# Performance work log

Measured on AMD Instinct MI355X. Metric: run time of the kernel, lower is better.

## Reference

```python
import jax, jax.numpy as jnp
from jax import lax
import numpy as np

B = 32768
H = 7
W = 7
EMB = 64
NUM_ACTIONS = 7
HIDDEN = 128
CNN_OUT = 64 * 3 * 3  # 576, from 7x7 input through the conv/pool stack


def setup_inputs() -> dict:
    key = jax.random.key(0)
    ks = jax.random.split(key, 20)
    frame = jax.random.randint(ks[0], (2, B, H, W, 3), 0, 11, dtype=jnp.int32)
    carried_col = jax.random.randint(ks[1], (2, B, 1), 0, 6, dtype=jnp.int32)
    carried_obj = jax.random.randint(ks[2], (2, B, 1), 0, 11, dtype=jnp.int32)

    def w(k, shape):
        return (jax.random.normal(k, shape, jnp.float32) * 0.05)

    return {
        "frame": frame,
        "carried_col": carried_col,
        "carried_obj": carried_obj,
        "conv1_w": w(ks[3], (16, 3, 2, 2)),  "conv1_b": jnp.zeros((16,), jnp.float32),
        "conv2_w": w(ks[4], (32, 16, 2, 2)), "conv2_b": jnp.zeros((32,), jnp.float32),
        "conv3_w": w(ks[5], (64, 32, 2, 2)), "conv3_b": jnp.zeros((64,), jnp.float32),
        "proj_w": w(ks[6], (EMB, CNN_OUT + 2)), "proj_b": jnp.zeros((EMB,), jnp.float32),
        "h1_w": w(ks[7], (HIDDEN, EMB * 2 + 4)), "h1_b": jnp.zeros((HIDDEN,), jnp.float32),
        "ln_g": jnp.ones((HIDDEN,), jnp.float32), "ln_b": jnp.zeros((HIDDEN,), jnp.float32),
        "h2_w": w(ks[8], (HIDDEN, HIDDEN)), "h2_b": jnp.zeros((HIDDEN,), jnp.float32),
        "h3_w": w(ks[9], (NUM_ACTIONS, HIDDEN)), "h3_b": jnp.zeros((NUM_ACTIONS,), jnp.float32),
    }


def _conv(x, wgt, b):
    # Conv2d(kernel=2, padding=1), NCHW
    y = lax.conv_general_dilated(x, wgt, (1, 1), [(1, 1), (1, 1)],
                                 dimension_numbers=("NCHW", "OIHW", "NCHW"))
    return y + b[None, :, None, None]


def _maxpool2(x):
    # MaxPool2d(2): window 2, stride 2, floor (VALID)
    return lax.reduce_window(x, -jnp.inf, lax.max, (1, 1, 2, 2), (1, 1, 2, 2), "VALID")


def _encode(fr, cc, co, p):
    x = fr.transpose(0, 3, 1, 2).astype(jnp.float32)  # [B,3,H,W]
    x = _maxpool2(jax.nn.relu(_conv(x, p["conv1_w"], p["conv1_b"])))  # [B,16,4,4]
    x = _maxpool2(jax.nn.relu(_conv(x, p["conv2_w"], p["conv2_b"])))  # [B,32,2,2]
    x = jax.nn.relu(_conv(x, p["conv3_w"], p["conv3_b"]))             # [B,64,3,3]
    feats = x.reshape(x.shape[0], -1)                                  # [B,576]
    carried = jnp.concatenate([cc, co], axis=-1).astype(jnp.float32)   # [B,2]
    comb = jnp.concatenate([feats, carried], axis=1)                   # [B,578]
    return jax.nn.relu(comb @ p["proj_w"].T + p["proj_b"])            # [B,64]


def _dir_pos(fr):
    # vectorized first-match of frame[...,0]==10 in row-major order
    b = fr.shape[0]
    mask = (fr[..., 0] == 10).reshape(b, -1)             # [B, H*W]
    has = jnp.any(mask, axis=-1)                         # [B]
    idx = jnp.argmax(mask, axis=-1)                      # first True (row-major)
    y = idx // W
    x = idx % W
    ch2 = fr[..., 2].reshape(b, -1)
    d_raw = jnp.take_along_axis(ch2, idx[:, None], axis=1)[:, 0] % 4
    d = jnp.where(has, d_raw, 0)                         # [B] int
    pos = jnp.stack([y.astype(jnp.float32) / (H - 1),
                     x.astype(jnp.float32) / (W - 1)], axis=-1)
    pos = jnp.where(has[:, None], pos, jnp.float32(0.5))  # [B,2]
    return d, pos


def _forward(frame, carried_col, carried_obj, p):
    curr_f, next_f = frame[0], frame[1]
    curr_emb = _encode(curr_f, carried_col[0], carried_obj[0], p)
    next_emb = _encode(next_f, carried_col[1], carried_obj[1], p)
    cd, cpos = _dir_pos(curr_f)
    nd, npos = _dir_pos(next_f)
    delta = ((nd - cd + 4) % 4).astype(jnp.float32)
    angle = delta * (2.0 * 3.14159 / 4.0)  # matches source constant
    dir_delta = jnp.stack([jnp.sin(angle), jnp.cos(angle)], axis=-1)  # [B,2]
    pos_delta = npos - cpos                                           # [B,2]
    comb = jnp.concatenate([curr_emb, next_emb, dir_delta, pos_delta], axis=-1)  # [B,132]
    h = comb @ p["h1_w"].T + p["h1_b"]
    mu = h.mean(-1, keepdims=True)
    var = ((h - mu) ** 2).mean(-1, keepdims=True)
    h = (h - mu) * lax.rsqrt(var + 1e-5) * p["ln_g"] + p["ln_b"]
    h = jax.nn.relu(h)  # dropout = identity in eval
    h = jax.nn.relu(h @ p["h2_w"].T + p["h2_b"])
    return h @ p["h3_w"].T + p["h3_b"]  # [B, num_actions]


def reference(frame, carried_col, carried_obj,
              conv1_w, conv1_b, conv2_w, conv2_b, conv3_w, conv3_b,
              proj_w, proj_b, h1_w, h1_b, ln_g, ln_b,
              h2_w, h2_b, h3_w, h3_b):
    p = dict(conv1_w=conv1_w, conv1_b=conv1_b, conv2_w=conv2_w, conv2_b=conv2_b,
             conv3_w=conv3_w, conv3_b=conv3_b, proj_w=proj_w, proj_b=proj_b,
             h1_w=h1_w, h1_b=h1_b, ln_g=ln_g, ln_b=ln_b,
             h2_w=h2_w, h2_b=h2_b, h3_w=h3_w, h3_b=h3_b)
    return _forward(frame, carried_col, carried_obj, p)
```

## Files before the change

kernel.cpp:

```cpp
#include <hip/hip_runtime.h>
#include <hip/hip_bf16.h>

#define BATCH 32768
#define NELEM 65536

typedef unsigned short u16;
typedef unsigned int u32;
typedef __attribute__((ext_vector_type(8))) short bf16x8;
typedef __attribute__((ext_vector_type(4))) float f32x4;

__device__ __forceinline__ float bf2f(u16 u) {
    union { u32 u; float f; } c; c.u = ((u32)u) << 16; return c.f;
}
__device__ __forceinline__ u16 f2bf(float f) {
    union { float f; u32 u; } c; c.f = f;
    u32 x = c.u;
    u32 r = (x + 0x7fffu + ((x >> 16) & 1u)) >> 16;
    return (u16)r;
}

__global__ __launch_bounds__(256) void k0_prep(const float* __restrict__ pw,
        const float* __restrict__ w2, const float* __restrict__ w3,
        const float* __restrict__ h2w, const float* __restrict__ h1w,
        const float* __restrict__ w1,
        u16* __restrict__ pwT, u16* __restrict__ w2r, u16* __restrict__ w3r,
        u16* __restrict__ h2hi, u16* __restrict__ h2lo,
        u16* __restrict__ h1hi, u16* __restrict__ h1lo,
        u16* __restrict__ w1hi, u16* __restrict__ w1lo) {
    int idx = blockIdx.x * 256 + threadIdx.x;
    if (idx < 38912) {
        int j = idx / 608, kk = idx - j * 608;
        float v = 0.f;
        if (kk < 576) {
            int p = kk >> 6, oc = kk & 63;
            v = pw[j * 578 + oc * 9 + p];
        } else if (kk < 578) {
            v = pw[j * 578 + kk];
        }
        pwT[idx] = f2bf(v);
    } else if (idx < 40960) {
        int i = idx - 38912;
        int oc = i >> 6, rem = i & 63, tap = rem >> 4, ic = rem & 15;
        w2r[i] = f2bf(w2[oc * 64 + ic * 4 + tap]);
    } else if (idx < 49152) {
        int i = idx - 40960;
        int oc = i >> 7, rem = i & 127, tap = rem >> 5, ic = rem & 31;
        w3r[i] = f2bf(w3[oc * 128 + ic * 4 + tap]);
    } else if (idx < 65536) {
        int i = idx - 49152;
        float v = h2w[i];
        u16 hi = f2bf(v);
        h2hi[i] = hi;
        h2lo[i] = f2bf(v - bf2f(hi));
    } else if (idx < 86016) {
        int i = idx - 65536;
        int j = i / 160, k = i - j * 160;
        float v = (k < 132) ? h1w[j * 132 + k] : 0.f;
        u16 hi = f2bf(v);
        h1hi[i] = hi;
        h1lo[i] = f2bf(v - bf2f(hi));
    } else if (idx < 86528) {
        int i = idx - 86016;
        int oc = i >> 5, k = i & 31;
        int ky = k >> 4, kx = (k >> 3) & 1, c = k & 7;
        float v = (c < 3) ? w1[oc * 12 + c * 4 + ky * 2 + kx] : 0.f;
        u16 hi = f2bf(v);
        w1hi[i] = hi;
        w1lo[i] = f2bf(v - bf2f(hi));
    }
}

__global__ __launch_bounds__(256) void k1_conv1_mfma(const int* __restrict__ frame,
        const u16* __restrict__ w1hi, const u16* __restrict__ w1lo,
        const float* __restrict__ b1, u16* __restrict__ pooled1b) {
    __shared__ u16 fr[16 * 656];
    int t = threadIdx.x;
    int e0 = blockIdx.x * 16;
    #pragma unroll
    for (int i = 0; i < 6; ++i) {
        int o = i * 256 + t;
        if (o < 1312) *(uint4*)(fr + o * 8) = make_uint4(0u, 0u, 0u, 0u);
    }
    __syncthreads();
    #pragma unroll
    for (int i = 0; i < 10; ++i) {
        int idx = i * 256 + t;
        if (idx < 2352) {
            int le = idx / 147, r = idx - le * 147;
            int cell = r / 3, c = r - cell * 3;
            int y = cell / 7, x = cell - y * 7;
            fr[le * 656 + (y + 1) * 72 + (x + 1) * 8 + c] = f2bf((float)frame[e0 * 147 + idx]);
        }
    }
    __syncthreads();
    int l = t & 63;
    int wv = t >> 6;
    int col = l & 15;
    int kg = l >> 4;
    bf16x8 bhi = *(const bf16x8*)(w1hi + col * 32 + kg * 8);
    bf16x8 blo = *(const bf16x8*)(w1lo + col * 32 + kg * 8);
    float bias = b1[col];
    int ky = kg >> 1, kx = kg & 1;
    bool writer = (kg < 2);
    #pragma unroll
    for (int q = 0; q < 4; ++q) {
        int le = wv * 4 + q;
        const u16* eb = fr + le * 656;
        u16* op = pooled1b + (size_t)(e0 + le) * 256;
        #pragma unroll
        for (int mt = 0; mt < 4; ++mt) {
            int posA = mt * 16 + col;
            int oy = posA >> 3, ox = posA & 7;
            bf16x8 a = *(const bf16x8*)(eb + (oy + ky) * 72 + (ox + kx) * 8);
            f32x4 acc = {0.f, 0.f, 0.f, 0.f};
            acc = __builtin_amdgcn_mfma_f32_16x16x32_bf16(a, bhi, acc, 0, 0, 0);
            acc = __builtin_amdgcn_mfma_f32_16x16x32_bf16(a, blo, acc, 0, 0, 0);
            float x0 = fmaxf(acc[0] + bias, 0.f);
            float x1 = fmaxf(acc[1] + bias, 0.f);
            float x2 = fmaxf(acc[2] + bias, 0.f);
            float x3 = fmaxf(acc[3] + bias, 0.f);
            float y0 = fmaxf(x0, x1);
            float y1 = fmaxf(x2, x3);
            float m0 = fmaxf(y0, __shfl_xor(y0, 32, 64));
            float m1 = fmaxf(y1, __shfl_xor(y1, 32, 64));
            if (writer) {
                op[(mt * 4 + kg * 2 + 0) * 16 + col] = f2bf(m0);
                op[(mt * 4 + kg * 2 + 1) * 16 + col] = f2bf(m1);
            }
        }
    }
}

#define K2_WAVES 4096
__global__ __launch_bounds__(256) void k2_conv2_mfma(const u16* __restrict__ pooled1b,
        const u16* __restrict__ w2r, const float* __restrict__ b2,
        u16* __restrict__ pooled2) {
    int t = threadIdx.x;
    int l = t & 63;
    int col = l & 15;
    int kg = l >> 4;
    int wv = (blockIdx.x * 256 + t) >> 6;

    bf16x8 bfrag[2][2];
    #pragma unroll
    for (int s = 0; s < 2; ++s)
        #pragma unroll
        for (int nt = 0; nt < 2; ++nt)
            bfrag[s][nt] = *(const bf16x8*)(w2r + (nt * 16 + col) * 64 + s * 32 + kg * 8);
    float bias[2] = { b2[col], b2[16 + col] };

    int oy = col >> 2, ox = col & 3;
    int aoff[2]; bool aok[2];
    #pragma unroll
    for (int s = 0; s < 2; ++s) {
        int tap = 2 * s + (kg >> 1);
        int ky = tap >> 1, kx = tap & 1;
        int iy = oy - 1 + ky, ix = ox - 1 + kx;
        aok[s] = (iy >= 0 && ix >= 0);
        aoff[s] = (iy * 4 + ix) * 16 + (kg & 1) * 8;
    }

    for (int e = wv; e < NELEM; e += K2_WAVES) {
        const u16* pbase = pooled1b + e * 256;
        bf16x8 a0 = {0,0,0,0,0,0,0,0}, a1 = {0,0,0,0,0,0,0,0};
        if (aok[0]) a0 = *(const bf16x8*)(pbase + aoff[0]);
        if (aok[1]) a1 = *(const bf16x8*)(pbase + aoff[1]);
        f32x4 acc0 = {0.f,0.f,0.f,0.f}, acc1 = {0.f,0.f,0.f,0.f};
        acc0 = __builtin_amdgcn_mfma_f32_16x16x32_bf16(a0, bfrag[0][0], acc0, 0, 0, 0);
        acc1 = __builtin_amdgcn_mfma_f32_16x16x32_bf16(a0, bfrag[0][1], acc1, 0, 0, 0);
        acc0 = __builtin_amdgcn_mfma_f32_16x16x32_bf16(a1, bfrag[1][0], acc0, 0, 0, 0);
        acc1 = __builtin_amdgcn_mfma_f32_16x16x32_bf16(a1, bfrag[1][1], acc1, 0, 0, 0);
        #pragma unroll
        for (int nt = 0; nt < 2; ++nt) {
            f32x4 acc = nt ? acc1 : acc0;
            float b = bias[nt];
            float m0 = fmaxf(fmaxf(acc[0] + b, 0.f), fmaxf(acc[1] + b, 0.f));
            float m1 = fmaxf(fmaxf(acc[2] + b, 0.f), fmaxf(acc[3] + b, 0.f));
            float p0 = fmaxf(m0, __shfl_xor(m0, 16, 64));
            float p1 = fmaxf(m1, __shfl_xor(m1, 16, 64));
            if ((kg & 1) == 0) {
                int q = (kg >> 1) * 2;
                u16* op = pooled2 + e * 128 + nt * 16 + col;
                op[q * 32]       = f2bf(p0);
                op[(q + 1) * 32] = f2bf(p1);
            }
        }
    }
}

__global__ __launch_bounds__(256) void k34_conv3_proj(const u16* __restrict__ pooled2,
        const u16* __restrict__ w3r, const float* __restrict__ b3,
        const int* __restrict__ ccol, const int* __restrict__ cobj,
        const u16* __restrict__ pwT, const float* __restrict__ pb,
        float* __restrict__ comb) {
    __shared__ u16 featL[32 * 640];
    __shared__ u16 p2L[32 * 128];
    int t = threadIdx.x;
    int l = t & 63;
    int col = l & 15;
    int kg = l >> 4;
    int wv = t >> 6;
    int e0 = blockIdx.x * 32;
    int colhi = col >> 3, collo = col & 7;

    {
        const uint4* src = (const uint4*)(pooled2 + (size_t)e0 * 128);
        uint4* dst = (uint4*)p2L;
        #pragma unroll
        for (int i = 0; i < 2; ++i) dst[i * 256 + t] = src[i * 256 + t];
    }
    __syncthreads();

    {
        bf16x8 bfrag[4][4];
        #pragma unroll
        for (int s = 0; s < 4; ++s)
            #pragma unroll
            for (int nt = 0; nt < 4; ++nt)
                bfrag[s][nt] = *(const bf16x8*)(w3r + (nt * 16 + col) * 128 + s * 32 + kg * 8);
        float bias[4];
        #pragma unroll
        for (int nt = 0; nt < 4; ++nt) bias[nt] = b3[nt * 16 + col];

        auto do_tile = [&](int i) {
            int m0 = i * 16;
            int m = m0 + col;
            u32 elem = (u32)(((unsigned long long)(u32)m * 954437177ull) >> 33);
            int p = m - (int)elem * 9;
            int oy = (p * 86) >> 8;
            int ox = p - 3 * oy;
            const u16* pbase = p2L + elem * 128 + kg * 8;
            f32x4 acc[4];
            #pragma unroll
            for (int nt = 0; nt < 4; ++nt) {
                acc[nt][0] = 0.f; acc[nt][1] = 0.f; acc[nt][2] = 0.f; acc[nt][3] = 0.f;
            }
            #pragma unroll
            for (int s = 0; s < 4; ++s) {
                int ky = s >> 1, kx = s & 1;
                int iy = oy - 1 + ky, ix = ox - 1 + kx;
                bf16x8 a = {0,0,0,0,0,0,0,0};
                if (iy >= 0 && iy <= 1 && ix >= 0 && ix <= 1)
                    a = *(const bf16x8*)(pbase + (iy * 2 + ix) * 32);
                #pragma unroll
                for (int nt = 0; nt < 4; ++nt)
                    acc[nt] = __builtin_amdgcn_mfma_f32_16x16x32_bf16(a, bfrag[s][nt], acc[nt], 0, 0, 0);
            }
            #pragma unroll
            for (int r = 0; r < 4; ++r) {
                int mr = m0 + kg * 4 + r;
                u32 er = (u32)(((unsigned long long)(u32)mr * 954437177ull) >> 33);
                int pr = mr - (int)er * 9;
                int e7 = (int)(er & 7u);
                u16* fb = featL + er * 640 + collo;
                #pragma unroll
                for (int nt = 0; nt < 4; ++nt) {
                    int blk = (pr * 8 + nt * 2 + colhi) ^ e7;
                    fb[blk * 8] = f2bf(fmaxf(acc[nt][r] + bias[nt], 0.f));
                }
            }
        };
        #pragma unroll
        for (int u = 0; u < 4; ++u) do_tile(wv + u * 4);
        if (wv < 2) do_tile(16 + wv);
    }
    if (t < 32) {
        union { u16 s[8]; uint4 q; } b;
        b.s[0] = f2bf((float)ccol[e0 + t]);
        b.s[1] = f2bf((float)cobj[e0 + t]);
        #pragma unroll
        for (int i = 2; i < 8; ++i) b.s[i] = 0;
        *(uint4*)(featL + t * 640 + (72 ^ (t & 7)) * 8) = b.q;
    }
    __syncthreads();

    int rh = wv & 1, nh = wv >> 1;
    int m0g = e0 + rh * 16;
    const u16* arowb = featL + (rh * 16 + col) * 640;
    int rx = col & 7;
    const u16* brow = pwT + (nh * 32 + col) * 608 + kg * 8;
    f32x4 acc0 = {0.f,0.f,0.f,0.f}, acc1 = {0.f,0.f,0.f,0.f};
    #pragma unroll
    for (int k0 = 0; k0 < 608; k0 += 32) {
        bf16x8 a;
        if (k0 + kg * 8 < 584) {
            int L = (k0 >> 3) + kg;
            a = *(const bf16x8*)(arowb + (L ^ rx) * 8);
        } else {
            #pragma unroll
            for (int j = 0; j < 8; ++j) a[j] = 0;
        }
        bf16x8 b0 = *(const bf16x8*)(brow + k0);
        bf16x8 b1 = *(const bf16x8*)(brow + 16 * 608 + k0);
        acc0 = __builtin_amdgcn_mfma_f32_16x16x32_bf16(a, b0, acc0, 0, 0, 0);
        acc1 = __builtin_amdgcn_mfma_f32_16x16x32_bf16(a, b1, acc1, 0, 0, 0);
    }
    float* outbase = (m0g < BATCH) ? (comb + (size_t)m0g * 160)
                                   : (comb + (size_t)(m0g - BATCH) * 160 + 64);
    #pragma unroll
    for (int nt = 0; nt < 2; ++nt) {
        int n = nh * 32 + nt * 16 + col;
        float pbv = pb[n];
        f32x4 acc = nt ? acc1 : acc0;
        #pragma unroll
        for (int r = 0; r < 4; ++r) {
            outbase[(kg * 4 + r) * 160 + n] = fmaxf(acc[r] + pbv, 0.f);
        }
    }
}

__global__ __launch_bounds__(256) void k5_extras(const int* __restrict__ frame,
        float* __restrict__ comb) {
    int b = blockIdx.x * 256 + threadIdx.x;
    int d[2]; float posy[2], posx[2];
    for (int f = 0; f < 2; ++f) {
        const int* fb = frame + (size_t)(f * BATCH + b) * 147;
        int idx = 49;
        for (int cell = 0; cell < 49; ++cell) {
            int v = fb[cell * 3];
            if (idx == 49 && v == 10) idx = cell;
        }
        if (idx < 49) {
            d[f] = fb[idx * 3 + 2] & 3;
            posy[f] = (float)(idx / 7) / 6.0f;
            posx[f] = (float)(idx % 7) / 6.0f;
        } else {
            d[f] = 0; posy[f] = 0.5f; posx[f] = 0.5f;
        }
    }
    int delta = (d[1] - d[0] + 4) & 3;
    const float ANG = (float)(2.0 * 3.14159 / 4.0);
    float angle = (float)delta * ANG;
    float4 o;
    o.x = sinf(angle);
    o.y = cosf(angle);
    o.z = posy[1] - posy[0];
    o.w = posx[1] - posx[0];
    float* cb = comb + (size_t)b * 160 + 128;
    *(float4*)cb = o;
    float4 z = make_float4(0.f, 0.f, 0.f, 0.f);
    #pragma unroll
    for (int i = 1; i < 8; ++i) *(float4*)(cb + i * 4) = z;
}

__device__ __forceinline__ void split8(const float* __restrict__ x,
                                       bf16x8& hi, bf16x8& lo) {
    #pragma unroll
    for (int j = 0; j < 8; ++j) {
        u16 h = f2bf(x[j]);
        hi[j] = (short)h;
        lo[j] = (short)f2bf(x[j] - bf2f(h));
    }
}

__global__ __launch_bounds__(256) void k6_h1_gemm(const float* __restrict__ in,
        const u16* __restrict__ whi, const u16* __restrict__ wlo,
        const float* __restrict__ bias, float* __restrict__ out) {
    int t = threadIdx.x;
    int l = t & 63;
    int col = l & 15;
    int kg = l >> 4;
    int m0 = blockIdx.x * 64 + (t >> 6) * 16;
    const float* arow = in + (size_t)(m0 + col) * 160 + kg * 8;
    const u16* bh = whi + col * 160 + kg * 8;
    const u16* bl = wlo + col * 160 + kg * 8;

    f32x4 acc[8];
    #pragma unroll
    for (int nt = 0; nt < 8; ++nt) {
        acc[nt][0] = 0.f; acc[nt][1] = 0.f; acc[nt][2] = 0.f; acc[nt][3] = 0.f;
    }
    #pragma unroll
    for (int s = 0; s < 5; ++s) {
        float x[8];
        #pragma unroll
        for (int j = 0; j < 8; ++j) x[j] = arow[s * 32 + j];
        bf16x8 ahi, alo;
        split8(x, ahi, alo);
        #pragma unroll
        for (int nt = 0; nt < 8; ++nt) {
            bf16x8 bhiF = *(const bf16x8*)(bh + nt * 2560 + s * 32);
            bf16x8 bloF = *(const bf16x8*)(bl + nt * 2560 + s * 32);
            acc[nt] = __builtin_amdgcn_mfma_f32_16x16x32_bf16(ahi, bhiF, acc[nt], 0, 0, 0);
            acc[nt] = __builtin_amdgcn_mfma_f32_16x16x32_bf16(alo, bhiF, acc[nt], 0, 0, 0);
            acc[nt] = __builtin_amdgcn_mfma_f32_16x16x32_bf16(ahi, bloF, acc[nt], 0, 0, 0);
        }
    }
    #pragma unroll
    for (int nt = 0; nt < 8; ++nt) {
        float bv = bias[nt * 16 + col];
        #pragma unroll
        for (int r = 0; r < 4; ++r) {
            int m = m0 + kg * 4 + r;
            out[m * 128 + nt * 16 + col] = acc[nt][r] + bv;
        }
    }
}

__global__ __launch_bounds__(256) void k6_ln(const float* __restrict__ h,
        const float* __restrict__ lng, const float* __restrict__ lnb,
        float* __restrict__ out) {
    int w = (blockIdx.x * 256 + threadIdx.x) >> 6;
    int l = threadIdx.x & 63;
    const float* row = h + (size_t)w * 128 + l * 2;
    float2 v = *(const float2*)row;
    float s = v.x + v.y;
    s += __shfl_xor(s, 1, 64);
    s += __shfl_xor(s, 2, 64);
    s += __shfl_xor(s, 4, 64);
    s += __shfl_xor(s, 8, 64);
    s += __shfl_xor(s, 16, 64);
    s += __shfl_xor(s, 32, 64);
    float mu = s * (1.0f / 128.0f);
    float d0 = v.x - mu, d1 = v.y - mu;
    float vs = d0 * d0 + d1 * d1;
    vs += __shfl_xor(vs, 1, 64);
    vs += __shfl_xor(vs, 2, 64);
    vs += __shfl_xor(vs, 4, 64);
    vs += __shfl_xor(vs, 8, 64);
    vs += __shfl_xor(vs, 16, 64);
    vs += __shfl_xor(vs, 32, 64);
    float rs = rsqrtf(vs * (1.0f / 128.0f) + 1e-5f);
    float2 o;
    o.x = fmaxf(d0 * rs * lng[l * 2]     + lnb[l * 2],     0.f);
    o.y = fmaxf(d1 * rs * lng[l * 2 + 1] + lnb[l * 2 + 1], 0.f);
    *(float2*)(out + (size_t)w * 128 + l * 2) = o;
}

__global__ __launch_bounds__(256) void k7_h2_mfma(const float* __restrict__ in,
        const u16* __restrict__ whi, const u16* __restrict__ wlo,
        const float* __restrict__ bias, float* __restrict__ out) {
    int t = threadIdx.x;
    int l = t & 63;
    int col = l & 15;
    int kg = l >> 4;
    int m0 = blockIdx.x * 64 + (t >> 6) * 16;
    const float* arow = in + (size_t)(m0 + col) * 128 + kg * 8;
    const u16* bh = whi + col * 128 + kg * 8;
    const u16* bl = wlo + col * 128 + kg * 8;

    f32x4 acc[8];
    #pragma unroll
    for (int nt = 0; nt < 8; ++nt) {
        acc[nt][0] = 0.f; acc[nt][1] = 0.f; acc[nt][2] = 0.f; acc[nt][3] = 0.f;
    }
    #pragma unroll
    for (int s = 0; s < 4; ++s) {
        float x[8];
        #pragma unroll
        for (int j = 0; j < 8; ++j) x[j] = arow[s * 32 + j];
        bf16x8 ahi, alo;
        split8(x, ahi, alo);
        #pragma unroll
        for (int nt = 0; nt < 8; ++nt) {
            bf16x8 bhiF = *(const bf16x8*)(bh + nt * 2048 + s * 32);
            bf16x8 bloF = *(const bf16x8*)(bl + nt * 2048 + s * 32);
            acc[nt] = __builtin_amdgcn_mfma_f32_16x16x32_bf16(ahi, bhiF, acc[nt], 0, 0, 0);
            acc[nt] = __builtin_amdgcn_mfma_f32_16x16x32_bf16(alo, bhiF, acc[nt], 0, 0, 0);
            acc[nt] = __builtin_amdgcn_mfma_f32_16x16x32_bf16(ahi, bloF, acc[nt], 0, 0, 0);
        }
    }
    #pragma unroll
    for (int nt = 0; nt < 8; ++nt) {
        float bv = bias[nt * 16 + col];
        #pragma unroll
        for (int r = 0; r < 4; ++r) {
            int m = m0 + kg * 4 + r;
            out[m * 128 + nt * 16 + col] = fmaxf(acc[nt][r] + bv, 0.f);
        }
    }
}

__global__ __launch_bounds__(256) void k8_h3(const float* __restrict__ in,
        const float* __restrict__ w, const float* __restrict__ bias,
        float* __restrict__ out) {
    int r = blockIdx.x * 256 + threadIdx.x;
    float acc[7];
    #pragma unroll
    for (int j = 0; j < 7; ++j) acc[j] = bias[j];
    const float* row = in + (size_t)r * 128;
    #pragma unroll 4
    for (int c = 0; c < 32; ++c) {
        float4 v = *(const float4*)(row + c * 4);
        #pragma unroll
        for (int j = 0; j < 7; ++j) {
            acc[j] += v.x * w[j * 128 + c * 4 + 0];
            acc[j] += v.y * w[j * 128 + c * 4 + 1];
            acc[j] += v.z * w[j * 128 + c * 4 + 2];
            acc[j] += v.w * w[j * 128 + c * 4 + 3];
        }
    }
    #pragma unroll
    for (int j = 0; j < 7; ++j) out[r * 7 + j] = acc[j];
}

extern "C" void kernel_launch(void* const* d_in, const int* in_sizes, int n_in,
                              void* d_out, int out_size, void* d_ws, size_t ws_size,
                              hipStream_t stream) {
    const int*   frame = (const int*)d_in[0];
    const int*   ccol  = (const int*)d_in[1];
    const int*   cobj  = (const int*)d_in[2];
    const float* w1    = (const float*)d_in[3];
    const float* b1    = (const float*)d_in[4];
    const float* w2    = (const float*)d_in[5];
    const float* b2    = (const float*)d_in[6];
    const float* w3    = (const float*)d_in[7];
    const float* b3    = (const float*)d_in[8];
    const float* pw    = (const float*)d_in[9];
    const float* pb    = (const float*)d_in[10];
    const float* h1w   = (const float*)d_in[11];
    const float* h1b   = (const float*)d_in[12];
    const float* lng   = (const float*)d_in[13];
    const float* lnb   = (const float*)d_in[14];
    const float* h2w   = (const float*)d_in[15];
    const float* h2b   = (const float*)d_in[16];
    const float* h3w   = (const float*)d_in[17];
    const float* h3b   = (const float*)d_in[18];
    float* out = (float*)d_out;

    char* ws = (char*)d_ws;
    u16*   pooled1b = (u16*)(ws + 0);
    float* comb     = (float*)(ws + 0);
    u16*   pooled2  = (u16*)(ws + 33554432);
    float* h1out    = (float*)(ws + 33554432);
    float* h2out    = (float*)(ws + 50331648);
    float* h1pre    = (float*)(ws + 95420416);
    u16*   pwT      = (u16*)(ws + 132120576);
    u16*   w2r      = (u16*)(ws + 132120576 + 131072);
    u16*   w3r      = (u16*)(ws + 132120576 + 139264);
    u16*   h2hi     = (u16*)(ws + 132120576 + 163840);
    u16*   h2lo     = (u16*)(ws + 132120576 + 196608);
    u16*   h1hi     = (u16*)(ws + 132120576 + 229376);
    u16*   h1lo     = (u16*)(ws + 132120576 + 270336);
    u16*   w1hi     = (u16*)(ws + 132120576 + 311296);
    u16*   w1lo     = (u16*)(ws + 132120576 + 312320);

    k0_prep<<<340, 256, 0, stream>>>(pw, w2, w3, h2w, h1w, w1,
                                     pwT, w2r, w3r, h2hi, h2lo, h1hi, h1lo,
                                     w1hi, w1lo);
    k1_conv1_mfma<<<4096, 256, 0, stream>>>(frame, w1hi, w1lo, b1, pooled1b);
    k2_conv2_mfma<<<1024, 256, 0, stream>>>(pooled1b, w2r, b2, pooled2);
    k34_conv3_proj<<<2048, 256, 0, stream>>>(pooled2, w3r, b3, ccol, cobj,
                                             pwT, pb, comb);
    k5_extras<<<128, 256, 0, stream>>>(frame, comb);
    k6_h1_gemm<<<512, 256, 0, stream>>>(comb, h1hi, h1lo, h1b, h1pre);
    k6_ln<<<8192, 256, 0, stream>>>(h1pre, lng, lnb, h1out);
    k7_h2_mfma<<<512, 256, 0, stream>>>(h1out, h2hi, h2lo, h2b, h2out);
    k8_h3<<<128, 256, 0, stream>>>(h2out, h3w, h3b, out);
}
```

Before: 260.3 us.

## Fuse conv1, conv2 and conv3+projection into one kernel using shared-memory intermediates

Merges the three separate conv kernels into one kernel in which each block handles 32 elements. The pooled conv1 and conv2 activations stay in LDS instead of being written to and re-read from global workspace. This is meant to remove global memory round-trips and two kernel launches. In exchange it uses about 48KB of LDS per block, which may reduce occupancy, and adds more barriers per block.

```diff
diff --git a/kernel.cpp b/kernel.cpp
--- a/kernel.cpp
+++ b/kernel.cpp
@@ -70,147 +70,133 @@
     }
 }
 
-__global__ __launch_bounds__(256) void k1_conv1_mfma(const int* __restrict__ frame,
+__global__ __launch_bounds__(256) void kconv_all(const int* __restrict__ frame,
         const u16* __restrict__ w1hi, const u16* __restrict__ w1lo,
-        const float* __restrict__ b1, u16* __restrict__ pooled1b) {
-    __shared__ u16 fr[16 * 656];
+        const float* __restrict__ b1,
+        const u16* __restrict__ w2r, const float* __restrict__ b2,
+        const u16* __restrict__ w3r, const float* __restrict__ b3,
+        const int* __restrict__ ccol, const int* __restrict__ cobj,
+        const u16* __restrict__ pwT, const float* __restrict__ pb,
+        float* __restrict__ comb) {
+    __shared__ u16 lds[24576];
+    u16* p2L   = lds;
+    u16* p1L   = lds + 4096;
+    u16* frL   = lds + 12288;
+    u16* featL = lds + 4096;
     int t = threadIdx.x;
-    int e0 = blockIdx.x * 16;
-    #pragma unroll
-    for (int i = 0; i < 6; ++i) {
-        int o = i * 256 + t;
-        if (o < 1312) *(uint4*)(fr + o * 8) = make_uint4(0u, 0u, 0u, 0u);
-    }
-    __syncthreads();
-    #pragma unroll
-    for (int i = 0; i < 10; ++i) {
-        int idx = i * 256 + t;
-        if (idx < 2352) {
-            int le = idx / 147, r = idx - le * 147;
-            int cell = r / 3, c = r - cell * 3;
-            int y = cell / 7, x = cell - y * 7;
-            fr[le * 656 + (y + 1) * 72 + (x + 1) * 8 + c] = f2bf((float)frame[e0 * 147 + idx]);
-        }
-    }
-    __syncthreads();
     int l = t & 63;
     int wv = t >> 6;
     int col = l & 15;
     int kg = l >> 4;
-    bf16x8 bhi = *(const bf16x8*)(w1hi + col * 32 + kg * 8);
-    bf16x8 blo = *(const bf16x8*)(w1lo + col * 32 + kg * 8);
-    float bias = b1[col];
-    int ky = kg >> 1, kx = kg & 1;
-    bool writer = (kg < 2);
-    #pragma unroll
-    for (int q = 0; q < 4; ++q) {
-        int le = wv * 4 + q;
-        const u16* eb = fr + le * 656;
-        u16* op = pooled1b + (size_t)(e0 + le) * 256;
-        #pragma unroll
-        for (int mt = 0; mt < 4; ++mt) {
-            int posA = mt * 16 + col;
-            int oy = posA >> 3, ox = posA & 7;
-            bf16x8 a = *(const bf16x8*)(eb + (oy + ky) * 72 + (ox + kx) * 8);
-            f32x4 acc = {0.f, 0.f, 0.f, 0.f};
-            acc = __builtin_amdgcn_mfma_f32_16x16x32_bf16(a, bhi, acc, 0, 0, 0);
-            acc = __builtin_amdgcn_mfma_f32_16x16x32_bf16(a, blo, acc, 0, 0, 0);
-            float x0 = fmaxf(acc[0] + bias, 0.f);
-            float x1 = fmaxf(acc[1] + bias, 0.f);
-            float x2 = fmaxf(acc[2] + bias, 0.f);
-            float x3 = fmaxf(acc[3] + bias, 0.f);
-            float y0 = fmaxf(x0, x1);
-            float y1 = fmaxf(x2, x3);
-            float m0 = fmaxf(y0, __shfl_xor(y0, 32, 64));
-            float m1 = fmaxf(y1, __shfl_xor(y1, 32, 64));
-            if (writer) {
-                op[(mt * 4 + kg * 2 + 0) * 16 + col] = f2bf(m0);
-                op[(mt * 4 + kg * 2 + 1) * 16 + col] = f2bf(m1);
+    int e0 = blockIdx.x * 32;
+
+    #pragma unroll
+    for (int i = 0; i < 6; ++i) {
+        int o = i * 256 + t;
+        if (o < 1312) *(uint4*)(frL + o * 8) = make_uint4(0u, 0u, 0u, 0u);
+    }
+
+    {
+        bf16x8 c1hi = *(const bf16x8*)(w1hi + col * 32 + kg * 8);
+        bf16x8 c1lo = *(const bf16x8*)(w1lo + col * 32 + kg * 8);
+        float c1b = b1[col];
+        int ky1 = kg >> 1, kx1 = kg & 1;
+        bool wr1 = (kg < 2);
+        for (int h = 0; h < 2; ++h) {
+            __syncthreads();
+            const int* fbase = frame + (size_t)(e0 + h * 16) * 147;
+            #pragma unroll
+            for (int i = 0; i < 10; ++i) {
+                int idx = i * 256 + t;
+                if (idx < 2352) {
+                    int le = idx / 147, r = idx - le * 147;
+                    int cell = r / 3, c = r - cell * 3;
+                    int y = cell / 7, x = cell - y * 7;
+                    frL[le * 656 + (y + 1) * 72 + (x + 1) * 8 + c] = f2bf((float)fbase[idx]);
+                }
             }
-        }
-    }
-}
-
-#define K2_WAVES 4096
-__global__ __launch_bounds__(256) void k2_conv2_mfma(const u16* __restrict__ pooled1b,
-        const u16* __restrict__ w2r, const float* __restrict__ b2,
-        u16* __restrict__ pooled2) {
-    int t = threadIdx.x;
-    int l = t & 63;
-    int col = l & 15;
-    int kg = l >> 4;
-    int wv = (blockIdx.x * 256 + t) >> 6;
-
-    bf16x8 bfrag[2][2];
-    #pragma unroll
-    for (int s = 0; s < 2; ++s)
-        #pragma unroll
-        for (int nt = 0; nt < 2; ++nt)
-            bfrag[s][nt] = *(const bf16x8*)(w2r + (nt * 16 + col) * 64 + s * 32 + kg * 8);
-    float bias[2] = { b2[col], b2[16 + col] };
-
-    int oy = col >> 2, ox = col & 3;
-    int aoff[2]; bool aok[2];
-    #pragma unroll
-    for (int s = 0; s < 2; ++s) {
-        int tap = 2 * s + (kg >> 1);
-        int ky = tap >> 1, kx = tap & 1;
-        int iy = oy - 1 + ky, ix = ox - 1 + kx;
-        aok[s] = (iy >= 0 && ix >= 0);
-        aoff[s] = (iy * 4 + ix) * 16 + (kg & 1) * 8;
-    }
-
-    for (int e = wv; e < NELEM; e += K2_WAVES) {
-        const u16* pbase = pooled1b + e * 256;
-        bf16x8 a0 = {0,0,0,0,0,0,0,0}, a1 = {0,0,0,0,0,0,0,0};
-        if (aok[0]) a0 = *(const bf16x8*)(pbase + aoff[0]);
-        if (aok[1]) a1 = *(const bf16x8*)(pbase + aoff[1]);
-        f32x4 acc0 = {0.f,0.f,0.f,0.f}, acc1 = {0.f,0.f,0.f,0.f};
-        acc0 = __builtin_amdgcn_mfma_f32_16x16x32_bf16(a0, bfrag[0][0], acc0, 0, 0, 0);
-        acc1 = __builtin_amdgcn_mfma_f32_16x16x32_bf16(a0, bfrag[0][1], acc1, 0, 0, 0);
-        acc0 = __builtin_amdgcn_mfma_f32_16x16x32_bf16(a1, bfrag[1][0], acc0, 0, 0, 0);
-        acc1 = __builtin_amdgcn_mfma_f32_16x16x32_bf16(a1, bfrag[1][1], acc1, 0, 0, 0);
-        #pragma unroll
-        for (int nt = 0; nt < 2; ++nt) {
-            f32x4 acc = nt ? acc1 : acc0;
-            float b = bias[nt];
-            float m0 = fmaxf(fmaxf(acc[0] + b, 0.f), fmaxf(acc[1] + b, 0.f));
-            float m1 = fmaxf(fmaxf(acc[2] + b, 0.f), fmaxf(acc[3] + b, 0.f));
-            float p0 = fmaxf(m0, __shfl_xor(m0, 16, 64));
-            float p1 = fmaxf(m1, __shfl_xor(m1, 16, 64));
-            if ((kg & 1) == 0) {
-                int q = (kg >> 1) * 2;
-                u16* op = pooled2 + e * 128 + nt * 16 + col;
-                op[q * 32]       = f2bf(p0);
-                op[(q + 1) * 32] = f2bf(p1);
+            __syncthreads();
+            #pragma unroll
+            for (int q = 0; q < 4; ++q) {
+                int le = wv * 4 + q;
+                const u16* eb = frL + le * 656;
+                u16* op = p1L + (h * 16 + le) * 256;
+                #pragma unroll
+                for (int mt = 0; mt < 4; ++mt) {
+                    int posA = mt * 16 + col;
+                    int oy = posA >> 3, ox = posA & 7;
+                    bf16x8 a = *(const bf16x8*)(eb + (oy + ky1) * 72 + (ox + kx1) * 8);
+                    f32x4 acc = {0.f, 0.f, 0.f, 0.f};
+                    acc = __builtin_amdgcn_mfma_f32_16x16x32_bf16(a, c1hi, acc, 0, 0, 0);
+                    acc = __builtin_amdgcn_mfma_f32_16x16x32_bf16(a, c1lo, acc, 0, 0, 0);
+                    float x0 = fmaxf(acc[0] + c1b, 0.f);
+                    float x1 = fmaxf(acc[1] + c1b, 0.f);
+                    float x2 = fmaxf(acc[2] + c1b, 0.f);
+                    float x3 = fmaxf(acc[3] + c1b, 0.f);
+                    float y0 = fmaxf(x0, x1);
+                    float y1 = fmaxf(x2, x3);
+                    float m0 = fmaxf(y0, __shfl_xor(y0, 32, 64));
+                    float m1 = fmaxf(y1, __shfl_xor(y1, 32, 64));
+                    if (wr1) {
+                        op[(mt * 4 + kg * 2 + 0) * 16 + col] = f2bf(m0);
+                        op[(mt * 4 + kg * 2 + 1) * 16 + col] = f2bf(m1);
+                    }
+                }
             }
         }
     }
-}
-
-__global__ __launch_bounds__(256) void k34_conv3_proj(const u16* __restrict__ pooled2,
-        const u16* __restrict__ w3r, const float* __restrict__ b3,
-        const int* __restrict__ ccol, const int* __restrict__ cobj,
-        const u16* __restrict__ pwT, const float* __restrict__ pb,
-        float* __restrict__ comb) {
-    __shared__ u16 featL[32 * 640];
-    __shared__ u16 p2L[32 * 128];
-    int t = threadIdx.x;
-    int l = t & 63;
-    int col = l & 15;
-    int kg = l >> 4;
-    int wv = t >> 6;
-    int e0 = blockIdx.x * 32;
+    __syncthreads();
+
+    {
+        bf16x8 bfrag[2][2];
+        #pragma unroll
+        for (int s = 0; s < 2; ++s)
+            #pragma unroll
+            for (int nt = 0; nt < 2; ++nt)
+                bfrag[s][nt] = *(const bf16x8*)(w2r + (nt * 16 + col) * 64 + s * 32 + kg * 8);
+        float bias2[2] = { b2[col], b2[16 + col] };
+        int oy = col >> 2, ox = col & 3;
+        int aoff[2]; bool aok[2];
+        #pragma unroll
+        for (int s = 0; s < 2; ++s) {
+            int tap = 2 * s + (kg >> 1);
+            int ky = tap >> 1, kx = tap & 1;
+            int iy = oy - 1 + ky, ix = ox - 1 + kx;
+            aok[s] = (iy >= 0 && ix >= 0);
+            aoff[s] = (iy * 4 + ix) * 16 + (kg & 1) * 8;
+        }
+        #pragma unroll
+        for (int q = 0; q < 8; ++q) {
+            int e = wv * 8 + q;
+            const u16* pbase = p1L + e * 256;
+            bf16x8 a0 = {0,0,0,0,0,0,0,0}, a1 = {0,0,0,0,0,0,0,0};
+            if (aok[0]) a0 = *(const bf16x8*)(pbase + aoff[0]);
+            if (aok[1]) a1 = *(const bf16x8*)(pbase + aoff[1]);
+            f32x4 acc0 = {0.f,0.f,0.f,0.f}, acc1 = {0.f,0.f,0.f,0.f};
+            acc0 = __builtin_amdgcn_mfma_f32_16x16x32_bf16(a0, bfrag[0][0], acc0, 0, 0, 0);
+            acc1 = __builtin_amdgcn_mfma_f32_16x16x32_bf16(a0, bfrag[0][1], acc1, 0, 0, 0);
+            acc0 = __builtin_amdgcn_mfma_f32_16x16x32_bf16(a1, bfrag[1][0], acc0, 0, 0, 0);
+            acc1 = __builtin_amdgcn_mfma_f32_16x16x32_bf16(a1, bfrag[1][1], acc1, 0, 0, 0);
+            #pragma unroll
+            for (int nt = 0; nt < 2; ++nt) {
+                f32x4 acc = nt ? acc1 : acc0;
+                float b = bias2[nt];
+                float m0 = fmaxf(fmaxf(acc[0] + b, 0.f), fmaxf(acc[1] + b, 0.f));
+                float m1 = fmaxf(fmaxf(acc[2] + b, 0.f), fmaxf(acc[3] + b, 0.f));
+                float p0 = fmaxf(m0, __shfl_xor(m0, 16, 64));
+                float p1 = fmaxf(m1, __shfl_xor(m1, 16, 64));
+                if ((kg & 1) == 0) {
+                    int qq = (kg >> 1) * 2;
+                    u16* op = p2L + e * 128 + nt * 16 + col;
+                    op[qq * 32]       = f2bf(p0);
+                    op[(qq + 1) * 32] = f2bf(p1);
+                }
+            }
+        }
+    }
+    __syncthreads();
+
     int colhi = col >> 3, collo = col & 7;
-
-    {
-        const uint4* src = (const uint4*)(pooled2 + (size_t)e0 * 128);
-        uint4* dst = (uint4*)p2L;
-        #pragma unroll
-        for (int i = 0; i < 2; ++i) dst[i * 256 + t] = src[i * 256 + t];
-    }
-    __syncthreads();
-
     {
         bf16x8 bfrag[4][4];
         #pragma unroll
@@ -519,9 +505,7 @@
     float* out = (float*)d_out;
 
     char* ws = (char*)d_ws;
-    u16*   pooled1b = (u16*)(ws + 0);
     float* comb     = (float*)(ws + 0);
-    u16*   pooled2  = (u16*)(ws + 33554432);
     float* h1out    = (float*)(ws + 33554432);
     float* h2out    = (float*)(ws + 50331648);
     float* h1pre    = (float*)(ws + 95420416);
@@ -538,10 +522,8 @@
     k0_prep<<<340, 256, 0, stream>>>(pw, w2, w3, h2w, h1w, w1,
                                      pwT, w2r, w3r, h2hi, h2lo, h1hi, h1lo,
                                      w1hi, w1lo);
-    k1_conv1_mfma<<<4096, 256, 0, stream>>>(frame, w1hi, w1lo, b1, pooled1b);
-    k2_conv2_mfma<<<1024, 256, 0, stream>>>(pooled1b, w2r, b2, pooled2);
-    k34_conv3_proj<<<2048, 256, 0, stream>>>(pooled2, w3r, b3, ccol, cobj,
-                                             pwT, pb, comb);
+    kconv_all<<<2048, 256, 0, stream>>>(frame, w1hi, w1lo, b1, w2r, b2,
+                                        w3r, b3, ccol, cobj, pwT, pb, comb);
     k5_extras<<<128, 256, 0, stream>>>(frame, comb);
     k6_h1_gemm<<<512, 256, 0, stream>>>(comb, h1hi, h1lo, h1b, h1pre);
     k6_ln<<<8192, 256, 0, stream>>>(h1pre, lng, lnb, h1out);
```

Measured after the change: 255.9 us. About the same (-1.7%).
